# Kernel optimization log

Measured on AMD Instinct MI355X. Metric: run time of the kernel, lower is better.

The kernel has to match this reference:

```python
import jax, jax.numpy as jnp
import numpy as np

N_CLASSES = 2
N_FEATURES = 100
PSI_DIM = 10
BATCH = 500000


def setup_inputs() -> dict:
    key = jax.random.key(0)
    k_x, k_ar, k_ai, k_pr, k_pi = jax.random.split(key, 5)
    x = jax.random.normal(k_x, (BATCH, N_FEATURES), dtype=jnp.float32)
    A_real = jax.random.normal(k_ar, (N_CLASSES, PSI_DIM, PSI_DIM, N_FEATURES), dtype=jnp.float32)
    A_imag = jax.random.normal(k_ai, (N_CLASSES, PSI_DIM, PSI_DIM, N_FEATURES), dtype=jnp.float32)
    psi_real = jax.random.normal(k_pr, (PSI_DIM,), dtype=jnp.float32)
    psi_imag = jax.random.normal(k_pi, (PSI_DIM,), dtype=jnp.float32)
    return {"x": x, "A_real": A_real, "A_imag": A_imag, "psi_real": psi_real, "psi_imag": psi_imag}


def reference(x, A_real, A_imag, psi_real, psi_imag):
    # result_{tk} = Re[ sum_{i,j,a} conj(psi)_i A_{kija} x_{ta} psi_j ]  (x is real)
    # P_{ij} = conj(psi)_i psi_j ; expand in real arithmetic to avoid complex tensors.
    P_re = jnp.outer(psi_real, psi_real) + jnp.outer(psi_imag, psi_imag)   # [i,j]
    P_im = jnp.outer(psi_real, psi_imag) - jnp.outer(psi_imag, psi_real)   # [i,j]
    # Re(M)_{ka} = sum_{ij} P_re A_real - P_im A_imag  -> tiny [2,100] matrix
    M_re = jnp.einsum('ij,kija->ka', P_re, A_real) - jnp.einsum('ij,kija->ka', P_im, A_imag)
    # out_{tk} = sum_a x_{ta} Re(M)_{ka} : memory-bound [t,100] x [100,2]
    return jnp.einsum('ta,ka->tk', x, M_re)
```

## Files before the change

kernel.cpp:

```cpp
#include <hip/hip_runtime.h>

#define NF    100
#define TILE  128
#define BLOCK 256
#define MAXF4 13

__global__ __launch_bounds__(128) void compute_M_kernel(
    const float* __restrict__ A_real, const float* __restrict__ A_imag,
    const float* __restrict__ psi_real, const float* __restrict__ psi_imag,
    float2* __restrict__ M2) {
  int a = threadIdx.x;
  if (a >= NF) return;
  float pr[10], pi[10];
#pragma unroll
  for (int i = 0; i < 10; ++i) { pr[i] = psi_real[i]; pi[i] = psi_imag[i]; }
  float m0 = 0.f, m1 = 0.f;
#pragma unroll
  for (int i = 0; i < 10; ++i) {
#pragma unroll
    for (int j = 0; j < 10; ++j) {
      float pre = pr[i] * pr[j] + pi[i] * pi[j];
      float pim = pr[i] * pi[j] - pi[i] * pr[j];
      int off = (i * 10 + j) * NF + a;
      m0 = fmaf(pre, A_real[off], m0);
      m0 = fmaf(-pim, A_imag[off], m0);
      m1 = fmaf(pre, A_real[off + 10000], m1);
      m1 = fmaf(-pim, A_imag[off + 10000], m1);
    }
  }
  M2[a] = make_float2(m0, m1);
}

__global__ __launch_bounds__(BLOCK) void out_kernel(
    const float4* __restrict__ x4, const float2* __restrict__ M2,
    float2* __restrict__ out, int batch) {
  __shared__ float4 xs4[TILE * 25];
  __shared__ float2 ms[NF];
  const int tid = threadIdx.x;
  const int t0 = blockIdx.x * TILE;
  int rows = batch - t0;
  if (rows > TILE) rows = TILE;
  const int n4 = rows * 25;

  if (tid < NF) ms[tid] = M2[tid];

  const float4* src = x4 + (long)t0 * 25;
  float4 v[MAXF4];
#pragma unroll
  for (int u = 0; u < MAXF4; ++u) {
    int f = tid + u * BLOCK;
    if (f < n4) v[u] = src[f];
  }
#pragma unroll
  for (int u = 0; u < MAXF4; ++u) {
    int f = tid + u * BLOCK;
    if (f < n4) xs4[f] = v[u];
  }
  __syncthreads();

  const int r = tid >> 1;
  const int h = tid & 1;
  const float2* xr = (const float2*)(xs4 + r * 25) + h * 25;
  const float2* mr = ms + h * 50;
  float a0 = 0.f, a1 = 0.f;
#pragma unroll
  for (int i = 0; i < 25; ++i) {
    float2 xv = xr[i];
    float2 mA = mr[2 * i];
    float2 mB = mr[2 * i + 1];
    a0 = fmaf(xv.x, mA.x, a0);
    a1 = fmaf(xv.x, mA.y, a1);
    a0 = fmaf(xv.y, mB.x, a0);
    a1 = fmaf(xv.y, mB.y, a1);
  }
  a0 += __shfl_xor(a0, 1);
  a1 += __shfl_xor(a1, 1);
  if (h == 0 && r < rows) out[t0 + r] = make_float2(a0, a1);
}

extern "C" void kernel_launch(void* const* d_in, const int* in_sizes, int n_in,
                              void* d_out, int out_size, void* d_ws, size_t ws_size,
                              hipStream_t stream) {
  const float* x  = (const float*)d_in[0];
  const float* Ar = (const float*)d_in[1];
  const float* Ai = (const float*)d_in[2];
  const float* pr = (const float*)d_in[3];
  const float* pi = (const float*)d_in[4];
  const int batch = in_sizes[0] / NF;

  float2* M2 = (float2*)d_ws;
  compute_M_kernel<<<1, 128, 0, stream>>>(Ar, Ai, pr, pi, M2);

  const int nblocks = (batch + TILE - 1) / TILE;
  out_kernel<<<nblocks, BLOCK, 0, stream>>>(
      (const float4*)x, (const float2*)M2, (float2*)d_out, batch);
}
```

Baseline: 352.1 us.

## Make output kernel persistent with double-buffered async global-to-LDS loads

Replaces the one-block-per-tile kernel with a persistent grid-stride kernel, capped at 768 blocks, that processes 64-row tiles. Each block uses `global_load_lds` to fetch the next tile straight into the other half of a double-buffered LDS area while it computes the current tile, so loads no longer pass through registers. The M coefficients are now read as float4. The aim is to overlap the memory stream with compute and keep more bytes in flight on a bandwidth-bound streaming reduction. In exchange, the thread-to-row mapping still assumes 128 rows, so half the threads do wasted reads, some of them past the current buffer. Correctness also depends on the barrier waiting for the async LDS loads to finish.

```diff
diff --git a/kernel.cpp b/kernel.cpp
--- a/kernel.cpp
+++ b/kernel.cpp
@@ -1,9 +1,12 @@
 #include <hip/hip_runtime.h>
+#include <stdint.h>
 
-#define NF    100
-#define TILE  128
-#define BLOCK 256
-#define MAXF4 13
+#define NF     100
+#define TILE   64
+#define BLOCK  256
+#define F4T    (TILE * 25)
+#define NLD    ((F4T + BLOCK - 1) / BLOCK)
+#define GRID   768
 
 __global__ __launch_bounds__(128) void compute_M_kernel(
     const float* __restrict__ A_real, const float* __restrict__ A_imag,
@@ -31,51 +34,72 @@
   M2[a] = make_float2(m0, m1);
 }
 
-__global__ __launch_bounds__(BLOCK) void out_kernel(
-    const float4* __restrict__ x4, const float2* __restrict__ M2,
-    float2* __restrict__ out, int batch) {
-  __shared__ float4 xs4[TILE * 25];
-  __shared__ float2 ms[NF];
-  const int tid = threadIdx.x;
-  const int t0 = blockIdx.x * TILE;
+__device__ __forceinline__ void stage_tile(const float4* __restrict__ x4,
+                                           float4* dst, int tile, int batch,
+                                           int tid) {
+  const int t0 = tile * TILE;
   int rows = batch - t0;
   if (rows > TILE) rows = TILE;
   const int n4 = rows * 25;
+  const float4* src = x4 + (size_t)t0 * 25;
+#pragma unroll
+  for (int u = 0; u < NLD; ++u) {
+    int f = u * BLOCK + tid;
+    if (f < n4) {
+      __builtin_amdgcn_global_load_lds(
+          (const __attribute__((address_space(1))) void*)(src + f),
+          (__attribute__((address_space(3))) void*)(dst + f), 16, 0, 0);
+    }
+  }
+}
 
-  if (tid < NF) ms[tid] = M2[tid];
+__global__ __launch_bounds__(BLOCK) void out_kernel(
+    const float4* __restrict__ x4, const float4* __restrict__ M4,
+    float2* __restrict__ out, int batch, int ntiles) {
+  __shared__ float4 xs[2][F4T];
+  __shared__ float4 ms[NF / 2];
 
-  const float4* src = x4 + (long)t0 * 25;
-  float4 v[MAXF4];
-#pragma unroll
-  for (int u = 0; u < MAXF4; ++u) {
-    int f = tid + u * BLOCK;
-    if (f < n4) v[u] = src[f];
-  }
-#pragma unroll
-  for (int u = 0; u < MAXF4; ++u) {
-    int f = tid + u * BLOCK;
-    if (f < n4) xs4[f] = v[u];
-  }
-  __syncthreads();
+  const int tid = threadIdx.x;
+  if (tid < NF / 2) ms[tid] = M4[tid];
 
   const int r = tid >> 1;
   const int h = tid & 1;
-  const float2* xr = (const float2*)(xs4 + r * 25) + h * 25;
-  const float2* mr = ms + h * 50;
-  float a0 = 0.f, a1 = 0.f;
+  const int stride = gridDim.x;
+
+  int tile = blockIdx.x;
+  if (tile >= ntiles) return;
+
+  stage_tile(x4, &xs[0][0], tile, batch, tid);
+  int buf = 0;
+
+  for (; tile < ntiles; tile += stride) {
+    __syncthreads();
+
+    const int nxt = tile + stride;
+    if (nxt < ntiles) stage_tile(x4, &xs[buf ^ 1][0], nxt, batch, tid);
+
+    const int t0 = tile * TILE;
+    int rows = batch - t0;
+    if (rows > TILE) rows = TILE;
+
+    const float2* xr = (const float2*)(&xs[buf][0] + (size_t)r * 25) + h * 25;
+    const float4* mr = ms + h * 25;
+    float a0 = 0.f, a1 = 0.f;
 #pragma unroll
-  for (int i = 0; i < 25; ++i) {
-    float2 xv = xr[i];
-    float2 mA = mr[2 * i];
-    float2 mB = mr[2 * i + 1];
-    a0 = fmaf(xv.x, mA.x, a0);
-    a1 = fmaf(xv.x, mA.y, a1);
-    a0 = fmaf(xv.y, mB.x, a0);
-    a1 = fmaf(xv.y, mB.y, a1);
+    for (int i = 0; i < 25; ++i) {
+      float2 xv = xr[i];
+      float4 m = mr[i];
+      a0 = fmaf(xv.x, m.x, a0);
+      a1 = fmaf(xv.x, m.y, a1);
+      a0 = fmaf(xv.y, m.z, a0);
+      a1 = fmaf(xv.y, m.w, a1);
+    }
+    a0 += __shfl_xor(a0, 1);
+    a1 += __shfl_xor(a1, 1);
+    if (h == 0 && r < rows) out[t0 + r] = make_float2(a0, a1);
+
+    buf ^= 1;
   }
-  a0 += __shfl_xor(a0, 1);
-  a1 += __shfl_xor(a1, 1);
-  if (h == 0 && r < rows) out[t0 + r] = make_float2(a0, a1);
 }
 
 extern "C" void kernel_launch(void* const* d_in, const int* in_sizes, int n_in,
@@ -91,7 +115,8 @@
   float2* M2 = (float2*)d_ws;
   compute_M_kernel<<<1, 128, 0, stream>>>(Ar, Ai, pr, pi, M2);
 
-  const int nblocks = (batch + TILE - 1) / TILE;
-  out_kernel<<<nblocks, BLOCK, 0, stream>>>(
-      (const float4*)x, (const float2*)M2, (float2*)d_out, batch);
+  const int ntiles = (batch + TILE - 1) / TILE;
+  const int grid = ntiles < GRID ? ntiles : GRID;
+  out_kernel<<<grid, BLOCK, 0, stream>>>(
+      (const float4*)x, (const float4*)M2, (float2*)d_out, batch, ntiles);
 }
```

Result: faster. 284.0 us (-19.4%).

## Fuse M computation into persistent triple-buffered kernel using async global-to-LDS loads

Applied to the files above, without the earlier changes.

Merges the M-reduction kernel into the main kernel, so each block recomputes M locally and keeps it in registers. The main kernel becomes persistent (grid capped at 512) and streams 64-row tiles of x through three LDS buffers with global_load_lds, prefetching two tiles ahead under a manual waitcnt and barrier. This targets the separate launch, the register round-trip of the staging copy and the exposed load latency. In exchange every block repeats the A reduction, and the grid is far smaller, which may limit bandwidth occupancy.

```diff
diff --git a/kernel.cpp b/kernel.cpp
--- a/kernel.cpp
+++ b/kernel.cpp
@@ -1,81 +1,108 @@
 #include <hip/hip_runtime.h>
 
-#define NF    100
-#define TILE  128
-#define BLOCK 256
-#define MAXF4 13
+#define NF      100
+#define BLOCK   128
+#define TILE    64
+#define F4T     (TILE * 25)
+#define NLD     13
+#define F4PAD   (NLD * BLOCK)
+#define NBUF    3
+#define MAXGRID 512
 
-__global__ __launch_bounds__(128) void compute_M_kernel(
+__device__ __forceinline__ void stage_tile(const float4* __restrict__ x4,
+                                           float4* dst, int f4base, int maxf4,
+                                           int tid) {
+#pragma unroll
+  for (int u = 0; u < NLD; ++u) {
+    int g = f4base + u * BLOCK + tid;
+    g = g > maxf4 ? maxf4 : g;
+    __builtin_amdgcn_global_load_lds(
+        (const __attribute__((address_space(1))) void*)(x4 + g),
+        (__attribute__((address_space(3))) void*)(dst + u * BLOCK + tid),
+        16, 0, 0);
+  }
+}
+
+#define WAITCNT_VM13_LGKM0 0x007D
+
+__global__ __launch_bounds__(BLOCK, 1) void fused_kernel(
+    const float4* __restrict__ x4,
     const float* __restrict__ A_real, const float* __restrict__ A_imag,
     const float* __restrict__ psi_real, const float* __restrict__ psi_imag,
-    float2* __restrict__ M2) {
-  int a = threadIdx.x;
-  if (a >= NF) return;
-  float pr[10], pi[10];
+    float2* __restrict__ out, int batch, int ntiles) {
+  __shared__ float4 xs[NBUF][F4PAD];
+  __shared__ __align__(16) float2 msl[NF];
+
+  const int tid = threadIdx.x;
+
+  if (tid < NF) {
+    const int a = tid;
+    float pr[10], pi[10];
 #pragma unroll
-  for (int i = 0; i < 10; ++i) { pr[i] = psi_real[i]; pi[i] = psi_imag[i]; }
-  float m0 = 0.f, m1 = 0.f;
+    for (int i = 0; i < 10; ++i) { pr[i] = psi_real[i]; pi[i] = psi_imag[i]; }
+    float m0 = 0.f, m1 = 0.f;
 #pragma unroll
-  for (int i = 0; i < 10; ++i) {
+    for (int i = 0; i < 10; ++i) {
 #pragma unroll
-    for (int j = 0; j < 10; ++j) {
-      float pre = pr[i] * pr[j] + pi[i] * pi[j];
-      float pim = pr[i] * pi[j] - pi[i] * pr[j];
-      int off = (i * 10 + j) * NF + a;
-      m0 = fmaf(pre, A_real[off], m0);
-      m0 = fmaf(-pim, A_imag[off], m0);
-      m1 = fmaf(pre, A_real[off + 10000], m1);
-      m1 = fmaf(-pim, A_imag[off + 10000], m1);
+      for (int j = 0; j < 10; ++j) {
+        float pre = pr[i] * pr[j] + pi[i] * pi[j];
+        float pim = pr[i] * pi[j] - pi[i] * pr[j];
+        int off = (i * 10 + j) * NF + a;
+        m0 = fmaf(pre, A_real[off], m0);
+        m0 = fmaf(-pim, A_imag[off], m0);
+        m1 = fmaf(pre, A_real[off + 10000], m1);
+        m1 = fmaf(-pim, A_imag[off + 10000], m1);
+      }
     }
-  }
-  M2[a] = make_float2(m0, m1);
-}
-
-__global__ __launch_bounds__(BLOCK) void out_kernel(
-    const float4* __restrict__ x4, const float2* __restrict__ M2,
-    float2* __restrict__ out, int batch) {
-  __shared__ float4 xs4[TILE * 25];
-  __shared__ float2 ms[NF];
-  const int tid = threadIdx.x;
-  const int t0 = blockIdx.x * TILE;
-  int rows = batch - t0;
-  if (rows > TILE) rows = TILE;
-  const int n4 = rows * 25;
-
-  if (tid < NF) ms[tid] = M2[tid];
-
-  const float4* src = x4 + (long)t0 * 25;
-  float4 v[MAXF4];
-#pragma unroll
-  for (int u = 0; u < MAXF4; ++u) {
-    int f = tid + u * BLOCK;
-    if (f < n4) v[u] = src[f];
-  }
-#pragma unroll
-  for (int u = 0; u < MAXF4; ++u) {
-    int f = tid + u * BLOCK;
-    if (f < n4) xs4[f] = v[u];
+    msl[a] = make_float2(m0, m1);
   }
   __syncthreads();
 
+  const int h = tid & 1;
   const int r = tid >> 1;
-  const int h = tid & 1;
-  const float2* xr = (const float2*)(xs4 + r * 25) + h * 25;
-  const float2* mr = ms + h * 50;
-  float a0 = 0.f, a1 = 0.f;
+  const float4* msl4 = (const float4*)msl;
+  float4 mreg[26];
 #pragma unroll
-  for (int i = 0; i < 25; ++i) {
-    float2 xv = xr[i];
-    float2 mA = mr[2 * i];
-    float2 mB = mr[2 * i + 1];
-    a0 = fmaf(xv.x, mA.x, a0);
-    a1 = fmaf(xv.x, mA.y, a1);
-    a0 = fmaf(xv.y, mB.x, a0);
-    a1 = fmaf(xv.y, mB.y, a1);
+  for (int j = 0; j < 26; ++j) mreg[j] = msl4[24 * h + j];
+
+  const int maxf4 = batch * 25 - 1;
+  const int stride = gridDim.x;
+
+  float4* b0 = &xs[0][0];
+  float4* b1 = &xs[1][0];
+  float4* b2 = &xs[2][0];
+
+  int t = blockIdx.x;
+  stage_tile(x4, b0, t * F4T, maxf4, tid);
+  stage_tile(x4, b1, (t + stride) * F4T, maxf4, tid);
+
+  for (; t < ntiles; t += stride) {
+    __builtin_amdgcn_s_waitcnt(WAITCNT_VM13_LGKM0);
+    __builtin_amdgcn_s_barrier();
+
+    stage_tile(x4, b2, (t + 2 * stride) * F4T, maxf4, tid);
+
+    const float4* xrow = b0 + r * 25 + (h ? 12 : 0);
+    float a0 = 0.f, a1 = 0.f;
+#pragma unroll
+    for (int j = 0; j < 13; ++j) {
+      if (j < 12 + h) {
+        float4 xv = xrow[j];
+        float4 mA = mreg[2 * j];
+        float4 mB = mreg[2 * j + 1];
+        a0 = fmaf(xv.x, mA.x, a0); a1 = fmaf(xv.x, mA.y, a1);
+        a0 = fmaf(xv.y, mA.z, a0); a1 = fmaf(xv.y, mA.w, a1);
+        a0 = fmaf(xv.z, mB.x, a0); a1 = fmaf(xv.z, mB.y, a1);
+        a0 = fmaf(xv.w, mB.z, a0); a1 = fmaf(xv.w, mB.w, a1);
+      }
+    }
+    a0 += __shfl_xor(a0, 1);
+    a1 += __shfl_xor(a1, 1);
+    const int t0 = t * TILE;
+    if (h == 0 && r < batch - t0) out[t0 + r] = make_float2(a0, a1);
+
+    float4* tmp = b0; b0 = b1; b1 = b2; b2 = tmp;
   }
-  a0 += __shfl_xor(a0, 1);
-  a1 += __shfl_xor(a1, 1);
-  if (h == 0 && r < rows) out[t0 + r] = make_float2(a0, a1);
 }
 
 extern "C" void kernel_launch(void* const* d_in, const int* in_sizes, int n_in,
@@ -88,10 +115,8 @@
   const float* pi = (const float*)d_in[4];
   const int batch = in_sizes[0] / NF;
 
-  float2* M2 = (float2*)d_ws;
-  compute_M_kernel<<<1, 128, 0, stream>>>(Ar, Ai, pr, pi, M2);
-
-  const int nblocks = (batch + TILE - 1) / TILE;
-  out_kernel<<<nblocks, BLOCK, 0, stream>>>(
-      (const float4*)x, (const float2*)M2, (float2*)d_out, batch);
+  const int ntiles = (batch + TILE - 1) / TILE;
+  const int grid = ntiles < MAXGRID ? ntiles : MAXGRID;
+  fused_kernel<<<grid, BLOCK, 0, stream>>>(
+      (const float4*)x, Ar, Ai, pr, pi, (float2*)d_out, batch, ntiles);
 }
```

Result: faster. 286.5 us (-18.6%).
